# Optimization experiments

Measured on AMD Instinct MI355X. Metric: run time of the kernel, lower is better.

## Reference

```python
import jax, jax.numpy as jnp
import numpy as np

ENC_H, DEC_H, ATTN = 1024, 1024, 512
B, S = 32, 4096


def setup_inputs() -> dict:
    key = jax.random.key(0)
    k1, k2, k3, k4, k5, k6 = jax.random.split(key, 6)
    decoder_state = jax.random.normal(k1, (B, DEC_H), dtype=jnp.float32)
    encoder_outputs = jax.random.normal(k2, (B, S, ENC_H), dtype=jnp.float32)
    mask = jax.random.randint(k3, (B, S), 0, 2, dtype=jnp.int32)
    W_h = jax.random.normal(k4, (ENC_H, ATTN), dtype=jnp.float32) / np.sqrt(ENC_H)
    W_s = jax.random.normal(k5, (DEC_H, ATTN), dtype=jnp.float32) / np.sqrt(DEC_H)
    v = jax.random.normal(k6, (ATTN,), dtype=jnp.float32) / np.sqrt(ATTN)
    return {"decoder_state": decoder_state, "encoder_outputs": encoder_outputs,
            "mask": mask, "W_h": W_h, "W_s": W_s, "v": v}


def reference(decoder_state, encoder_outputs, mask, W_h, W_s, v):
    # proj_enc: (B, S, A), proj_dec: (B, 1, A)
    proj_enc = jnp.einsum('bse,ea->bsa', encoder_outputs, W_h)
    proj_dec = jnp.einsum('bd,da->ba', decoder_state, W_s)[:, None, :]
    # scores: (B, S) = v^T tanh(W_h h_j + W_s s_i)
    scores = jnp.einsum('bsa,a->bs', jnp.tanh(proj_enc + proj_dec), v)
    neg_inf = jnp.finfo(scores.dtype).min
    scores = jnp.where(mask == 0, neg_inf, scores)
    weights = jax.nn.softmax(scores, axis=-1)  # (B, S)
    context = jnp.einsum('bs,bse->be', weights, encoder_outputs)  # (B, ENC_H)
    return context, weights
```

## Files before the change

### kernel.cpp

```cpp
#include <hip/hip_runtime.h>
#include <hip/hip_bf16.h>
#include <float.h>
#include <math.h>

#define NB 32
#define NS 4096
#define NE 1024
#define ND 1024
#define NA 512

typedef __attribute__((ext_vector_type(4))) float f32x4;
typedef __attribute__((ext_vector_type(8))) short short8;
typedef __attribute__((ext_vector_type(4))) short short4v;

static __device__ __forceinline__ ushort f2bf(float f){
    union { float f; unsigned int u; } x; x.f = f;
    unsigned int u = x.u + 0x7fffu + ((x.u >> 16) & 1u);
    return (ushort)(u >> 16);
}

__global__ __launch_bounds__(256) void k_prep_wht(const float* __restrict__ Wh,
                                                  ushort* __restrict__ WT){
    int i = blockIdx.x * 256 + threadIdx.x;
    int k = i >> 9, a = i & 511;
    WT[a * 1024 + k] = f2bf(Wh[i]);
}

__global__ __launch_bounds__(512) void k_projdec(const float* __restrict__ dec,
                                                 const float* __restrict__ Ws,
                                                 float* __restrict__ pdp){
    int b = blockIdx.x >> 2, kc = blockIdx.x & 3;
    int a = threadIdx.x;
    const float* dp = dec + b * ND + kc * 256;
    const float* wp = Ws + (size_t)(kc * 256) * NA + a;
    float acc = 0.f;
    #pragma unroll 4
    for (int k = 0; k < 256; k++) acc += dp[k] * wp[(size_t)k * NA];
    pdp[(kc * NB + b) * NA + a] = acc;
}

__global__ __launch_bounds__(512, 4) void k_scores(const float* __restrict__ E,
                                                   const ushort* __restrict__ WT,
                                                   const float* __restrict__ pdp,
                                                   const float* __restrict__ v,
                                                   float* __restrict__ scores){
    const int t = threadIdx.x;
    const int wave = t >> 6, lane = t & 63;
    const int grp = lane >> 4, l15 = lane & 15;
    const int b = blockIdx.x >> 6;
    const int s0 = (blockIdx.x & 63) << 6;

    __shared__ __align__(16) ushort bft[2][64 * 64];
    __shared__ float sc[64][8];

    const int sr = t >> 3, scg = t & 7;
    const float* gsrc = E + ((size_t)(b * NS + s0 + sr)) * NE + scg * 8;
    const unsigned swb = (unsigned)(sr * 128 + ((scg ^ (sr & 7)) << 4));

    f32x4 stlo, sthi;

    f32x4 acc[4][4];
    f32x4 zero; zero[0]=0.f; zero[1]=0.f; zero[2]=0.f; zero[3]=0.f;
    #pragma unroll
    for (int m = 0; m < 4; m++)
        #pragma unroll
        for (int n = 0; n < 4; n++) acc[m][n] = zero;

    auto stage_load = [&](int it){
        const f32x4* p = (const f32x4*)(gsrc + it * 64);
        stlo = p[0]; sthi = p[1];
    };
    auto stage_write = [&](int buf){
        short8 h;
        #pragma unroll
        for (int e = 0; e < 4; e++){
            h[e]     = (short)f2bf(stlo[e]);
            h[e + 4] = (short)f2bf(sthi[e]);
        }
        *(short8*)((char*)&bft[buf][0] + swb) = h;
    };

    const int cb = wave * 64 + l15;

    stage_load(0);
    asm volatile("s_waitcnt vmcnt(0)" ::: "memory");
    stage_write(0);
    __builtin_amdgcn_s_barrier();

    for (int it = 0; it < 16; ++it){
        short8 wt[2][4];
        const ushort* wbase = WT + it * 64 + grp * 8;
        #pragma unroll
        for (int kk = 0; kk < 2; kk++)
            #pragma unroll
            for (int n = 0; n < 4; n++)
                wt[kk][n] = *(const short8*)(wbase + (size_t)(cb + n * 16) * 1024 + kk * 32);
        __builtin_amdgcn_sched_barrier(0);

        if (it < 15) stage_load(it + 1);
        __builtin_amdgcn_sched_barrier(0);

        const char* base = (const char*)&bft[it & 1][0];
        #pragma unroll
        for (int kk = 0; kk < 2; kk++){
            #pragma unroll
            for (int m = 0; m < 4; m++){
                const int r = m * 16 + l15;
                const int g = kk * 4 + grp;
                short8 af = *(const short8*)(base + r * 128 + (((g ^ (r & 7)) << 4)));
                #pragma unroll
                for (int n = 0; n < 4; n++)
                    acc[m][n] = __builtin_amdgcn_mfma_f32_16x16x32_bf16(af, wt[kk][n], acc[m][n], 0, 0, 0);
            }
        }
        __builtin_amdgcn_sched_barrier(0);

        if (it < 15){
            asm volatile("s_waitcnt vmcnt(0)" ::: "memory");
            stage_write((it + 1) & 1);
        }
        __builtin_amdgcn_s_barrier();
    }

    float pdc[4], vc[4];
    #pragma unroll
    for (int n = 0; n < 4; n++){
        int c = wave * 64 + n * 16 + l15;
        float p = 0.f;
        #pragma unroll
        for (int kc = 0; kc < 4; kc++) p += pdp[(kc * NB + b) * NA + c];
        pdc[n] = p;
        vc[n] = v[c];
    }
    #pragma unroll
    for (int m = 0; m < 4; m++){
        #pragma unroll
        for (int j = 0; j < 4; j++){
            float s = 0.f;
            #pragma unroll
            for (int n = 0; n < 4; n++) s += tanhf(acc[m][n][j] + pdc[n]) * vc[n];
            s += __shfl_xor(s, 1);
            s += __shfl_xor(s, 2);
            s += __shfl_xor(s, 4);
            s += __shfl_xor(s, 8);
            if (l15 == 0) sc[m * 16 + grp * 4 + j][wave] = s;
        }
    }
    __syncthreads();
    if (t < 64){
        float s = 0.f;
        #pragma unroll
        for (int w = 0; w < 8; w++) s += sc[t][w];
        scores[b * NS + s0 + t] = s;
    }
}

__global__ __launch_bounds__(256) void k_softmax(const float* __restrict__ scores,
                                                 const int* __restrict__ mask,
                                                 float* __restrict__ weights){
    int b = blockIdx.x, t = threadIdx.x;
    __shared__ float red[8];
    float vals[16];
    float mx = -FLT_MAX;
    #pragma unroll
    for (int i = 0; i < 16; i++){
        int s = i * 256 + t;
        float x = scores[b * NS + s];
        x = (mask[b * NS + s] != 0) ? x : -FLT_MAX;
        vals[i] = x;
        mx = fmaxf(mx, x);
    }
    #pragma unroll
    for (int off = 32; off; off >>= 1) mx = fmaxf(mx, __shfl_xor(mx, off));
    int wv = t >> 6;
    if ((t & 63) == 0) red[wv] = mx;
    __syncthreads();
    mx = fmaxf(fmaxf(red[0], red[1]), fmaxf(red[2], red[3]));
    float sum = 0.f;
    #pragma unroll
    for (int i = 0; i < 16; i++){ vals[i] = __expf(vals[i] - mx); sum += vals[i]; }
    #pragma unroll
    for (int off = 32; off; off >>= 1) sum += __shfl_xor(sum, off);
    if ((t & 63) == 0) red[4 + wv] = sum;
    __syncthreads();
    sum = red[4] + red[5] + red[6] + red[7];
    float inv = 1.f / sum;
    #pragma unroll
    for (int i = 0; i < 16; i++) weights[b * NS + i * 256 + t] = vals[i] * inv;
}

__global__ __launch_bounds__(1024) void k_context(const float* __restrict__ E,
                                                  const float* __restrict__ weights,
                                                  float* __restrict__ part){
    int b = blockIdx.x >> 3, ch = blockIdx.x & 7;
    int t = threadIdx.x;
    int h = t >> 8, tg = t & 255;
    __shared__ float wsm[512];
    __shared__ __align__(16) f32x4 red[4][256];
    if (t < 512) wsm[t] = weights[b * NS + ch * 512 + t];
    __syncthreads();
    const f32x4* Ep = (const f32x4*)(E + ((size_t)b * NS + ch * 512 + h * 128) * NE) + tg;
    f32x4 acc; acc[0]=0.f; acc[1]=0.f; acc[2]=0.f; acc[3]=0.f;
    #pragma unroll 4
    for (int s = 0; s < 128; s++){
        f32x4 e = Ep[(size_t)s * 256];
        float w = wsm[h * 128 + s];
        acc[0] += w * e[0]; acc[1] += w * e[1];
        acc[2] += w * e[2]; acc[3] += w * e[3];
    }
    red[h][tg] = acc;
    __syncthreads();
    if (h == 0){
        f32x4 a0 = red[0][tg], a1 = red[1][tg], a2 = red[2][tg], a3 = red[3][tg];
        f32x4 s;
        s[0] = a0[0]+a1[0]+a2[0]+a3[0];
        s[1] = a0[1]+a1[1]+a2[1]+a3[1];
        s[2] = a0[2]+a1[2]+a2[2]+a3[2];
        s[3] = a0[3]+a1[3]+a2[3]+a3[3];
        *(f32x4*)(part + ((size_t)(b * 8 + ch)) * NE + tg * 4) = s;
    }
}

__global__ __launch_bounds__(256) void k_reduce_ctx(const float* __restrict__ part,
                                                    float* __restrict__ ctx){
    int i = blockIdx.x * 256 + threadIdx.x;
    int b = i >> 10, e = i & 1023;
    float s = 0.f;
    #pragma unroll
    for (int ch = 0; ch < 8; ch++) s += part[((size_t)(b * 8 + ch)) * NE + e];
    ctx[i] = s;
}

extern "C" void kernel_launch(void* const* d_in, const int* in_sizes, int n_in,
                              void* d_out, int out_size, void* d_ws, size_t ws_size,
                              hipStream_t stream){
    const float* dec  = (const float*)d_in[0];
    const float* E    = (const float*)d_in[1];
    const int*   mask = (const int*)d_in[2];
    const float* Wh   = (const float*)d_in[3];
    const float* Ws   = (const float*)d_in[4];
    const float* v    = (const float*)d_in[5];
    float* ctx = (float*)d_out;
    float* weights = (float*)d_out + NB * NE;

    char* ws = (char*)d_ws;
    ushort* WT   = (ushort*)ws;
    float*  part = (float*)ws;
    float*  pdp  = (float*)(ws + (1 << 20));
    float*  scr  = (float*)(ws + (1 << 20) + (256 << 10));

    k_prep_wht<<<2048, 256, 0, stream>>>(Wh, WT);
    k_projdec<<<128, 512, 0, stream>>>(dec, Ws, pdp);
    k_scores<<<2048, 512, 0, stream>>>(E, WT, pdp, v, scr);
    k_softmax<<<32, 256, 0, stream>>>(scr, mask, weights);
    k_context<<<256, 1024, 0, stream>>>(E, weights, part);
    k_reduce_ctx<<<128, 256, 0, stream>>>(part, ctx);
}
```

Baseline: 413.3 us.

## Retile score GEMM to 256-row blocks with fragment-ordered weights and split N

```diff
diff --git a/kernel.cpp b/kernel.cpp
--- a/kernel.cpp
+++ b/kernel.cpp
@@ -11,7 +11,6 @@
 
 typedef __attribute__((ext_vector_type(4))) float f32x4;
 typedef __attribute__((ext_vector_type(8))) short short8;
-typedef __attribute__((ext_vector_type(4))) short short4v;
 
 static __device__ __forceinline__ ushort f2bf(float f){
     union { float f; unsigned int u; } x; x.f = f;
@@ -19,11 +18,16 @@
     return (ushort)(u >> 16);
 }
 
-__global__ __launch_bounds__(256) void k_prep_wht(const float* __restrict__ Wh,
-                                                  ushort* __restrict__ WT){
+__global__ __launch_bounds__(256) void k_prep_wtf(const float* __restrict__ Wh,
+                                                  ushort* __restrict__ WTf){
     int i = blockIdx.x * 256 + threadIdx.x;
-    int k = i >> 9, a = i & 511;
-    WT[a * 1024 + k] = f2bf(Wh[i]);
+    int e = i & 7;
+    int lane = (i >> 3) & 63;
+    int ng = (i >> 9) & 31;
+    int s = i >> 14;
+    int k = s * 32 + (lane >> 4) * 8 + e;
+    int col = ng * 16 + (lane & 15);
+    WTf[i] = f2bf(Wh[k * NA + col]);
 }
 
 __global__ __launch_bounds__(512) void k_projdec(const float* __restrict__ dec,
@@ -39,25 +43,27 @@
     pdp[(kc * NB + b) * NA + a] = acc;
 }
 
-__global__ __launch_bounds__(512, 4) void k_scores(const float* __restrict__ E,
-                                                   const ushort* __restrict__ WT,
-                                                   const float* __restrict__ pdp,
-                                                   const float* __restrict__ v,
-                                                   float* __restrict__ scores){
+__global__ __launch_bounds__(1024, 4) void k_scores(const float* __restrict__ E,
+                                                    const ushort* __restrict__ WTf,
+                                                    const float* __restrict__ v,
+                                                    float* __restrict__ scrp){
     const int t = threadIdx.x;
-    const int wave = t >> 6, lane = t & 63;
-    const int grp = lane >> 4, l15 = lane & 15;
-    const int b = blockIdx.x >> 6;
-    const int s0 = (blockIdx.x & 63) << 6;
-
-    __shared__ __align__(16) ushort bft[2][64 * 64];
-    __shared__ float sc[64][8];
-
-    const int sr = t >> 3, scg = t & 7;
-    const float* gsrc = E + ((size_t)(b * NS + s0 + sr)) * NE + scg * 8;
-    const unsigned swb = (unsigned)(sr * 128 + ((scg ^ (sr & 7)) << 4));
-
-    f32x4 stlo, sthi;
+    const int lane = t & 63, w = t >> 6;
+    const int l15 = lane & 15, grp = lane >> 4;
+    const int wm = w >> 2, wn = w & 3;
+
+    const int bid = blockIdx.x;
+    const int xcd = bid & 7, slot = bid >> 3;
+    const int mblk = xcd * 64 + (slot >> 1);
+    const int bn = slot & 1;
+    const int m0 = mblk << 8;
+
+    __shared__ __align__(16) ushort bft[2][256 * 64];
+    __shared__ float sc[256][4];
+
+    const int sr = t >> 2, sq = t & 3;
+    const float* gsrc = E + (size_t)(m0 + sr) * NE + sq * 16;
+    const unsigned wb0 = (unsigned)(sr * 128 + ((sq * 32) ^ ((sr & 7) << 4)));
 
     f32x4 acc[4][4];
     f32x4 zero; zero[0]=0.f; zero[1]=0.f; zero[2]=0.f; zero[3]=0.f;
@@ -66,66 +72,171 @@
         #pragma unroll
         for (int n = 0; n < 4; n++) acc[m][n] = zero;
 
+    f32x4 st[4];
     auto stage_load = [&](int it){
         const f32x4* p = (const f32x4*)(gsrc + it * 64);
-        stlo = p[0]; sthi = p[1];
+        st[0] = p[0]; st[1] = p[1]; st[2] = p[2]; st[3] = p[3];
     };
     auto stage_write = [&](int buf){
-        short8 h;
+        short8 h0, h1;
         #pragma unroll
         for (int e = 0; e < 4; e++){
-            h[e]     = (short)f2bf(stlo[e]);
-            h[e + 4] = (short)f2bf(sthi[e]);
-        }
-        *(short8*)((char*)&bft[buf][0] + swb) = h;
-    };
-
-    const int cb = wave * 64 + l15;
-
-    stage_load(0);
-    asm volatile("s_waitcnt vmcnt(0)" ::: "memory");
-    stage_write(0);
-    __builtin_amdgcn_s_barrier();
-
-    for (int it = 0; it < 16; ++it){
-        short8 wt[2][4];
-        const ushort* wbase = WT + it * 64 + grp * 8;
-        #pragma unroll
-        for (int kk = 0; kk < 2; kk++)
+            h0[e]     = (short)f2bf(st[0][e]);
+            h0[e + 4] = (short)f2bf(st[1][e]);
+            h1[e]     = (short)f2bf(st[2][e]);
+            h1[e + 4] = (short)f2bf(st[3][e]);
+        }
+        char* base = (char*)&bft[buf][0];
+        *(short8*)(base + wb0)        = h0;
+        *(short8*)(base + (wb0 ^ 16)) = h1;
+    };
+
+    const ushort* wtf0 = WTf + ((size_t)(bn * 16 + wn * 4) * 64 + lane) * 8;
+
+    auto compute_kk = [&](int buf, int kk, short8 (&wt)[4]){
+        const char* base = (const char*)&bft[buf][0];
+        #pragma unroll
+        for (int m = 0; m < 4; m++){
+            const int row = wm * 64 + m * 16 + l15;
+            short8 af = *(const short8*)(base + row * 128 + (((kk * 4 + grp) * 16) ^ ((row & 7) << 4)));
             #pragma unroll
             for (int n = 0; n < 4; n++)
-                wt[kk][n] = *(const short8*)(wbase + (size_t)(cb + n * 16) * 1024 + kk * 32);
-        __builtin_amdgcn_sched_barrier(0);
-
+                acc[m][n] = __builtin_amdgcn_mfma_f32_16x16x32_bf16(af, wt[n], acc[m][n], 0, 0, 0);
+        }
+    };
+
+    stage_load(0);
+    stage_write(0);
+    asm volatile("s_waitcnt lgkmcnt(0)" ::: "memory");
+    __builtin_amdgcn_s_barrier();
+
+    for (int it = 0; it < 16; ++it){
+        const int buf = it & 1;
+        short8 wt0[4], wt1[4];
+        const ushort* wp0 = wtf0 + (size_t)(it * 2) * 16384;
+        #pragma unroll
+        for (int n = 0; n < 4; n++) wt0[n] = *(const short8*)(wp0 + n * 512);
+        #pragma unroll
+        for (int n = 0; n < 4; n++) wt1[n] = *(const short8*)(wp0 + 16384 + n * 512);
+        __builtin_amdgcn_sched_barrier(0);
         if (it < 15) stage_load(it + 1);
         __builtin_amdgcn_sched_barrier(0);
-
-        const char* base = (const char*)&bft[it & 1][0];
-        #pragma unroll
-        for (int kk = 0; kk < 2; kk++){
+        compute_kk(buf, 0, wt0);
+        compute_kk(buf, 1, wt1);
+        __builtin_amdgcn_sched_barrier(0);
+        if (it < 15) stage_write(buf ^ 1);
+        asm volatile("s_waitcnt lgkmcnt(0)" ::: "memory");
+        __builtin_amdgcn_s_barrier();
+    }
+
+    float vc[4];
+    #pragma unroll
+    for (int n = 0; n < 4; n++) vc[n] = v[bn * 256 + wn * 64 + n * 16 + l15];
+    #pragma unroll
+    for (int m = 0; m < 4; m++){
+        #pragma unroll
+        for (int j = 0; j < 4; j++){
+            float s = 0.f;
             #pragma unroll
-            for (int m = 0; m < 4; m++){
-                const int r = m * 16 + l15;
-                const int g = kk * 4 + grp;
-                short8 af = *(const short8*)(base + r * 128 + (((g ^ (r & 7)) << 4)));
-                #pragma unroll
-                for (int n = 0; n < 4; n++)
-                    acc[m][n] = __builtin_amdgcn_mfma_f32_16x16x32_bf16(af, wt[kk][n], acc[m][n], 0, 0, 0);
-            }
-        }
-        __builtin_amdgcn_sched_barrier(0);
-
-        if (it < 15){
-            asm volatile("s_waitcnt vmcnt(0)" ::: "memory");
-            stage_write((it + 1) & 1);
-        }
+            for (int n = 0; n < 4; n++) s += acc[m][n][j] * 0.f + acc[m][n][j], s = s;
+        }
+    }
+    (void)vc;
+    (void)scrp;
+}
+
+__global__ __launch_bounds__(1024, 4) void k_scores_full(const float* __restrict__ E,
+                                                         const ushort* __restrict__ WTf,
+                                                         const float* __restrict__ pdp,
+                                                         const float* __restrict__ v,
+                                                         float* __restrict__ scrp){
+    const int t = threadIdx.x;
+    const int lane = t & 63, w = t >> 6;
+    const int l15 = lane & 15, grp = lane >> 4;
+    const int wm = w >> 2, wn = w & 3;
+
+    const int bid = blockIdx.x;
+    const int xcd = bid & 7, slot = bid >> 3;
+    const int mblk = xcd * 64 + (slot >> 1);
+    const int bn = slot & 1;
+    const int m0 = mblk << 8;
+    const int b = mblk >> 4;
+
+    __shared__ __align__(16) ushort bft[2][256 * 64];
+    __shared__ float sc[256][4];
+
+    const int sr = t >> 2, sq = t & 3;
+    const float* gsrc = E + (size_t)(m0 + sr) * NE + sq * 16;
+    const unsigned wb0 = (unsigned)(sr * 128 + ((sq * 32) ^ ((sr & 7) << 4)));
+
+    f32x4 acc[4][4];
+    f32x4 zero; zero[0]=0.f; zero[1]=0.f; zero[2]=0.f; zero[3]=0.f;
+    #pragma unroll
+    for (int m = 0; m < 4; m++)
+        #pragma unroll
+        for (int n = 0; n < 4; n++) acc[m][n] = zero;
+
+    f32x4 st[4];
+    auto stage_load = [&](int it){
+        const f32x4* p = (const f32x4*)(gsrc + it * 64);
+        st[0] = p[0]; st[1] = p[1]; st[2] = p[2]; st[3] = p[3];
+    };
+    auto stage_write = [&](int buf){
+        short8 h0, h1;
+        #pragma unroll
+        for (int e = 0; e < 4; e++){
+            h0[e]     = (short)f2bf(st[0][e]);
+            h0[e + 4] = (short)f2bf(st[1][e]);
+            h1[e]     = (short)f2bf(st[2][e]);
+            h1[e + 4] = (short)f2bf(st[3][e]);
+        }
+        char* base = (char*)&bft[buf][0];
+        *(short8*)(base + wb0)        = h0;
+        *(short8*)(base + (wb0 ^ 16)) = h1;
+    };
+
+    const ushort* wtf0 = WTf + ((size_t)(bn * 16 + wn * 4) * 64 + lane) * 8;
+
+    auto compute_kk = [&](int buf, int kk, short8 (&wt)[4]){
+        const char* base = (const char*)&bft[buf][0];
+        #pragma unroll
+        for (int m = 0; m < 4; m++){
+            const int row = wm * 64 + m * 16 + l15;
+            short8 af = *(const short8*)(base + row * 128 + (((kk * 4 + grp) * 16) ^ ((row & 7) << 4)));
+            #pragma unroll
+            for (int n = 0; n < 4; n++)
+                acc[m][n] = __builtin_amdgcn_mfma_f32_16x16x32_bf16(af, wt[n], acc[m][n], 0, 0, 0);
+        }
+    };
+
+    stage_load(0);
+    stage_write(0);
+    asm volatile("s_waitcnt lgkmcnt(0)" ::: "memory");
+    __builtin_amdgcn_s_barrier();
+
+    for (int it = 0; it < 16; ++it){
+        const int buf = it & 1;
+        short8 wt0[4], wt1[4];
+        const ushort* wp0 = wtf0 + (size_t)(it * 2) * 16384;
+        #pragma unroll
+        for (int n = 0; n < 4; n++) wt0[n] = *(const short8*)(wp0 + n * 512);
+        #pragma unroll
+        for (int n = 0; n < 4; n++) wt1[n] = *(const short8*)(wp0 + 16384 + n * 512);
+        __builtin_amdgcn_sched_barrier(0);
+        if (it < 15) stage_load(it + 1);
+        __builtin_amdgcn_sched_barrier(0);
+        compute_kk(buf, 0, wt0);
+        compute_kk(buf, 1, wt1);
+        __builtin_amdgcn_sched_barrier(0);
+        if (it < 15) stage_write(buf ^ 1);
+        asm volatile("s_waitcnt lgkmcnt(0)" ::: "memory");
         __builtin_amdgcn_s_barrier();
     }
 
     float pdc[4], vc[4];
     #pragma unroll
     for (int n = 0; n < 4; n++){
-        int c = wave * 64 + n * 16 + l15;
+        int c = bn * 256 + wn * 64 + n * 16 + l15;
         float p = 0.f;
         #pragma unroll
         for (int kc = 0; kc < 4; kc++) p += pdp[(kc * NB + b) * NA + c];
@@ -143,19 +254,15 @@
             s += __shfl_xor(s, 2);
             s += __shfl_xor(s, 4);
             s += __shfl_xor(s, 8);
-            if (l15 == 0) sc[m * 16 + grp * 4 + j][wave] = s;
-        }
-    }
-    __syncthreads();
-    if (t < 64){
-        float s = 0.f;
-        #pragma unroll
-        for (int w = 0; w < 8; w++) s += sc[t][w];
-        scores[b * NS + s0 + t] = s;
-    }
-}
-
-__global__ __launch_bounds__(256) void k_softmax(const float* __restrict__ scores,
+            if (l15 == 0) sc[wm * 64 + m * 16 + grp * 4 + j][wn] = s;
+        }
+    }
+    __syncthreads();
+    if (t < 256)
+        scrp[(size_t)bn * (NB * NS) + m0 + t] = sc[t][0] + sc[t][1] + sc[t][2] + sc[t][3];
+}
+
+__global__ __launch_bounds__(256) void k_softmax(const float* __restrict__ scrp,
                                                  const int* __restrict__ mask,
                                                  float* __restrict__ weights){
     int b = blockIdx.x, t = threadIdx.x;
@@ -165,7 +272,7 @@
     #pragma unroll
     for (int i = 0; i < 16; i++){
         int s = i * 256 + t;
-        float x = scores[b * NS + s];
+        float x = scrp[b * NS + s] + scrp[(size_t)(NB * NS) + b * NS + s];
         x = (mask[b * NS + s] != 0) ? x : -FLT_MAX;
         vals[i] = x;
         mx = fmaxf(mx, x);
@@ -244,15 +351,15 @@
     float* weights = (float*)d_out + NB * NE;
 
     char* ws = (char*)d_ws;
-    ushort* WT   = (ushort*)ws;
+    ushort* WTf  = (ushort*)ws;
     float*  part = (float*)ws;
     float*  pdp  = (float*)(ws + (1 << 20));
-    float*  scr  = (float*)(ws + (1 << 20) + (256 << 10));
-
-    k_prep_wht<<<2048, 256, 0, stream>>>(Wh, WT);
+    float*  scrp = (float*)(ws + (1 << 20) + (256 << 10));
+
+    k_prep_wtf<<<2048, 256, 0, stream>>>(Wh, WTf);
     k_projdec<<<128, 512, 0, stream>>>(dec, Ws, pdp);
-    k_scores<<<2048, 512, 0, stream>>>(E, WT, pdp, v, scr);
-    k_softmax<<<32, 256, 0, stream>>>(scr, mask, weights);
+    k_scores_full<<<1024, 1024, 0, stream>>>(E, WTf, pdp, v, scrp);
+    k_softmax<<<32, 256, 0, stream>>>(scrp, mask, weights);
     k_context<<<256, 1024, 0, stream>>>(E, weights, part);
     k_reduce_ctx<<<128, 256, 0, stream>>>(part, ctx);
 }
```

New measurement: 440.0 us. +6.5%, slower.
